# Performance work log

Measured on AMD Instinct MI355X. Metric: run time of the kernel, lower is better.

The kernel has to match this reference:

```python
import jax, jax.numpy as jnp
import numpy as np
from jax import lax

B, L, C = 128, 16384, 12      # batch, signal length, ECG channels
D = 128                        # latent_size
K, STRIDE = 64, 64             # encoder conv
TI, TO, TIG = 64, 8, 0         # timesteps_in / out / ignore


def setup_inputs() -> dict:
    key = jax.random.key(0)
    ks = jax.random.split(key, 7)
    s = 0.05
    X = jax.random.normal(ks[0], (B, L, C), jnp.float32)
    conv_w = jax.random.normal(ks[1], (D, C, K), jnp.float32) * s
    conv_b = jnp.zeros((D,), jnp.float32)
    W_ih = jax.random.normal(ks[2], (3 * D, D), jnp.float32) * s
    W_hh = jax.random.normal(ks[3], (3 * D, D), jnp.float32) * s
    b_ih = jnp.zeros((3 * D,), jnp.float32)
    b_hh = jnp.zeros((3 * D,), jnp.float32)
    pred_W = jax.random.normal(ks[4], (TO, D, D), jnp.float32) * s
    pred_b = jnp.zeros((TO, D), jnp.float32)
    return {"X": X, "conv_w": conv_w, "conv_b": conv_b, "W_ih": W_ih,
            "W_hh": W_hh, "b_ih": b_ih, "b_hh": b_hh,
            "pred_W": pred_W, "pred_b": pred_b}


def _gru(enc, W_ih, W_hh, b_ih, b_hh):
    # enc: [T, B, D] -> context [T, B, D], final hidden [B, D]
    def step(h, xt):
        gi = xt @ W_ih.T + b_ih              # [B, 3D]
        gh = h @ W_hh.T + b_hh
        ir, iz, inn = jnp.split(gi, 3, axis=-1)
        hr, hz, hn = jnp.split(gh, 3, axis=-1)
        r = jax.nn.sigmoid(ir + hr)
        z = jax.nn.sigmoid(iz + hz)
        n = jnp.tanh(inn + r * hn)
        h_new = (1.0 - z) * n + z * h
        return h_new, h_new
    h0 = jnp.zeros((enc.shape[1], enc.shape[2]), enc.dtype)
    hT, ctx = lax.scan(step, h0, enc)
    return ctx, hT


def reference(X, conv_w, conv_b, W_ih, W_hh, b_ih, b_hh, pred_W, pred_b):
    # X: [B, L, C] -> [B, C, L]
    x = X.transpose(0, 2, 1)
    z = lax.conv_general_dilated(x, conv_w, (STRIDE,), 'VALID',
                                 dimension_numbers=('NCH', 'OIH', 'NCH'))
    z = jax.nn.relu(z + conv_b[None, :, None])     # [B, D, T]
    enc = z.transpose(2, 0, 1)                     # [T, B, D]
    ctx, hT = _gru(enc, W_ih, W_hh, b_ih, b_hh)    # [T, B, D]

    T = enc.shape[0]
    S = T - TI - (TO + TIG + 1)                    # prediction steps per offset
    ctx_s = ctx[TI:TI + S]                         # [S, B, D]
    # predictor per offset i: ctx_s @ W[i].T + b[i]  -> [O, S, B, D]
    pred = jnp.einsum('sbd,oed->osbe', ctx_s, pred_W) + pred_b[:, None, None, :]
    # encoded targets enc[TI+i+1 : TI+i+1+S] for each offset i -> [O, S, B, D]
    idx = TI + 1 + jnp.arange(TO)[:, None] + jnp.arange(S)[None, :]
    tgt = enc[idx]
    # scores[o,s,b,c] = <encoded_latent[b], pred_latent[c]>
    scores = jnp.einsum('osbd,oscd->osbc', tgt, pred)
    logsm = jax.nn.log_softmax(scores, axis=-1)
    diag = jnp.diagonal(logsm, axis1=-2, axis2=-1)  # [O, S, B]
    denom = jnp.float32(B * TO * S)
    loss = -jnp.sum(diag) / denom
    correct = jnp.sum(jnp.argmax(logsm, axis=-2) == jnp.arange(B)[None, None, :])
    accuracy = correct.astype(jnp.float32) / denom
    hidden = hT[None]                               # [1, B, D]
    return accuracy, loss, hidden
```

## Files before the change

### kernel.cpp

```cpp
#include <hip/hip_runtime.h>
#include <math.h>

typedef __attribute__((ext_vector_type(8))) short bf16x8;
typedef __attribute__((ext_vector_type(4))) float f32x4;

#define Bdim 128
#define Cdim 12
#define Ddim 128
#define Tdim 256
#define TOn  8
#define TIn  64
#define Sn   183
#define DENOMF 187392.0f
#define NEG_INF -3.402823466e38f

#define OFFB_ENC 0
#define OFFB_CTX 8388608
#define OFFB_GI  16777216
#define OFFB_BCT 67108864
#define OFFB_WT  67305472
#define OFFB_LP  67403776
#define OFFB_CP  67409632
#define OFFB_WHP 67415488
#define OFFB_PWB 67513792

__device__ __forceinline__ float frcp(float x) { return __builtin_amdgcn_rcpf(x); }

__device__ __forceinline__ unsigned short f2b(float x) {
    unsigned int u = __builtin_bit_cast(unsigned int, x);
    u += 0x7FFFu + ((u >> 16) & 1u);
    return (unsigned short)(u >> 16);
}
__device__ __forceinline__ unsigned int pk2(float a, float b) {
    return (unsigned int)f2b(a) | ((unsigned int)f2b(b) << 16);
}

__device__ __forceinline__ uint4 ldg4u_pin(const unsigned int* p) {
    uint4 r;
    asm volatile("global_load_dwordx4 %0, %1, off\n\ts_waitcnt vmcnt(0)"
                 : "=v"(r) : "v"(p) : "memory");
    return r;
}

__device__ __forceinline__ void dot2b(float& acc, unsigned int a, unsigned int b) {
    asm("v_dot2_f32_bf16 %0, %1, %2, %0" : "+v"(acc) : "v"(a), "v"(b));
}

__device__ __forceinline__ float dpp_xor1(float x) {
    return __builtin_bit_cast(float, __builtin_amdgcn_mov_dpp(
        __builtin_bit_cast(int, x), 0xB1, 0xF, 0xF, true));
}
__device__ __forceinline__ float dpp_xor2(float x) {
    return __builtin_bit_cast(float, __builtin_amdgcn_mov_dpp(
        __builtin_bit_cast(int, x), 0x4E, 0xF, 0xF, true));
}

__global__ __launch_bounds__(256) void k_prep(const float* __restrict__ conv_w,
                                              unsigned short* __restrict__ BcT,
                                              const float* __restrict__ W_ih,
                                              unsigned short* __restrict__ Wt,
                                              const float* __restrict__ W_hh,
                                              unsigned int* __restrict__ Whp,
                                              const float* __restrict__ pW,
                                              unsigned short* __restrict__ pWb) {
    int id = blockIdx.x * 256 + threadIdx.x;
    if (id < 128 * 768) {
        int d = id / 768, klin = id % 768;
        int kt = klin / 12, c = klin % 12;
        BcT[id] = f2b(conv_w[d * 768 + c * 64 + kt]);
    }
    if (id < 384 * 128) Wt[id] = f2b(W_ih[id]);
    if (id < 384 * 64) {
        int row = id >> 6, k2 = id & 63;
        Whp[id] = pk2(W_hh[row * 128 + 2 * k2], W_hh[row * 128 + 2 * k2 + 1]);
    }
    if (id < 8 * 128 * 128) pWb[id] = f2b(pW[id]);
}

__global__ __launch_bounds__(256) void k_conv(const float* __restrict__ X,
                                              const unsigned short* __restrict__ BcT,
                                              const float* __restrict__ conv_b,
                                              unsigned short* __restrict__ encb) {
    const int t = blockIdx.x;
    __shared__ __align__(16) char As[16384];
    __shared__ __align__(16) char Bs[16384];
    const int tid = threadIdx.x;
    const int lane = tid & 63, wid = tid >> 6;
    const int wy = wid >> 1, wx = wid & 1;
    const int g = lane >> 4, ln = lane & 15;

    f32x4 acc[4][4];
#pragma unroll
    for (int i = 0; i < 4; ++i)
#pragma unroll
        for (int j = 0; j < 4; ++j) acc[i][j] = (f32x4){0.f, 0.f, 0.f, 0.f};

    for (int kc = 0; kc < 768; kc += 64) {
        __syncthreads();
#pragma unroll
        for (int it = 0; it < 4; ++it) {
            int G = tid + it * 256;
            int r = G >> 3, go = G & 7;
            const float* src = X + (size_t)r * (16384 * 12) + t * 768 + kc + go * 8;
            float4 f0 = *(const float4*)src;
            float4 f1 = *(const float4*)(src + 4);
            uint4 w; w.x = pk2(f0.x, f0.y); w.y = pk2(f0.z, f0.w);
            w.z = pk2(f1.x, f1.y); w.w = pk2(f1.z, f1.w);
            *(uint4*)(As + (r * 8 + (go ^ (r & 7))) * 16) = w;
            uint4 v = *(const uint4*)(BcT + (size_t)r * 768 + kc + go * 8);
            *(uint4*)(Bs + (r * 8 + (go ^ (r & 7))) * 16) = v;
        }
        __syncthreads();
#pragma unroll
        for (int ks = 0; ks < 2; ++ks) {
            bf16x8 af[4], bfr[4];
            const int kb = ks * 64 + g * 16;
#pragma unroll
            for (int mi = 0; mi < 4; ++mi) {
                int r = wy * 64 + mi * 16 + ln;
                af[mi] = *(const bf16x8*)(As + r * 128 + (kb ^ ((r & 7) << 4)));
            }
#pragma unroll
            for (int ni = 0; ni < 4; ++ni) {
                int r = wx * 64 + ni * 16 + ln;
                bfr[ni] = *(const bf16x8*)(Bs + r * 128 + (kb ^ ((r & 7) << 4)));
            }
#pragma unroll
            for (int mi = 0; mi < 4; ++mi)
#pragma unroll
                for (int ni = 0; ni < 4; ++ni)
                    acc[mi][ni] = __builtin_amdgcn_mfma_f32_16x16x32_bf16(af[mi], bfr[ni], acc[mi][ni], 0, 0, 0);
        }
    }
    float cb[4];
#pragma unroll
    for (int ni = 0; ni < 4; ++ni) cb[ni] = conv_b[wx * 64 + ni * 16 + ln];
    unsigned short* dst = encb + (size_t)t * (128 * 128);
#pragma unroll
    for (int mi = 0; mi < 4; ++mi)
#pragma unroll
        for (int jj = 0; jj < 4; ++jj) {
            int b = wy * 64 + mi * 16 + g * 4 + jj;
#pragma unroll
            for (int ni = 0; ni < 4; ++ni) {
                int d = wx * 64 + ni * 16 + ln;
                dst[b * 128 + d] = f2b(fmaxf(acc[mi][ni][jj] + cb[ni], 0.f));
            }
        }
}

__global__ __launch_bounds__(256) void k_gi(const unsigned short* __restrict__ encb,
                                            const unsigned short* __restrict__ Wt,
                                            const float* __restrict__ b_ih,
                                            const float* __restrict__ b_hh,
                                            float* __restrict__ gi) {
    const int mt = blockIdx.x, nt = blockIdx.y;
    __shared__ __align__(16) char As[32768];
    __shared__ __align__(16) char Bs[32768];
    const int tid = threadIdx.x;
    const int lane = tid & 63, wid = tid >> 6;
    const int wy = wid >> 1, wx = wid & 1;
    const int g = lane >> 4, ln = lane & 15;

    {
        const unsigned short* asrc = encb + (size_t)mt * (128 * 128);
        const unsigned short* bsrc = Wt + (size_t)nt * (128 * 128);
#pragma unroll
        for (int it = 0; it < 8; ++it) {
            int G = tid + it * 256;
            int r = G >> 4, go = G & 15;
            *(uint4*)(As + (r * 16 + (go ^ (r & 7))) * 16) = *(const uint4*)(asrc + r * 128 + go * 8);
            *(uint4*)(Bs + (r * 16 + (go ^ (r & 7))) * 16) = *(const uint4*)(bsrc + r * 128 + go * 8);
        }
    }
    __syncthreads();

    f32x4 acc[4][4];
#pragma unroll
    for (int i = 0; i < 4; ++i)
#pragma unroll
        for (int j = 0; j < 4; ++j) acc[i][j] = (f32x4){0.f, 0.f, 0.f, 0.f};
#pragma unroll
    for (int ks = 0; ks < 4; ++ks) {
        bf16x8 af[4], bfr[4];
        const int kb = ks * 64 + g * 16;
#pragma unroll
        for (int mi = 0; mi < 4; ++mi) {
            int r = wy * 64 + mi * 16 + ln;
            af[mi] = *(const bf16x8*)(As + r * 256 + (kb ^ ((r & 7) << 4)));
        }
#pragma unroll
        for (int ni = 0; ni < 4; ++ni) {
            int r = wx * 64 + ni * 16 + ln;
            bfr[ni] = *(const bf16x8*)(Bs + r * 256 + (kb ^ ((r & 7) << 4)));
        }
#pragma unroll
        for (int mi = 0; mi < 4; ++mi)
#pragma unroll
            for (int ni = 0; ni < 4; ++ni)
                acc[mi][ni] = __builtin_amdgcn_mfma_f32_16x16x32_bf16(af[mi], bfr[ni], acc[mi][ni], 0, 0, 0);
    }
    float bv[4];
#pragma unroll
    for (int ni = 0; ni < 4; ++ni) {
        int n = nt * 128 + wx * 64 + ni * 16 + ln;
        bv[ni] = b_ih[n] + (n < 256 ? b_hh[n] : 0.f);
    }
#pragma unroll
    for (int mi = 0; mi < 4; ++mi)
#pragma unroll
        for (int jj = 0; jj < 4; ++jj) {
            int m = mt * 128 + wy * 64 + mi * 16 + g * 4 + jj;
#pragma unroll
            for (int ni = 0; ni < 4; ++ni) {
                int n = nt * 128 + wx * 64 + ni * 16 + ln;
                gi[(size_t)m * 384 + n] = acc[mi][ni][jj] + bv[ni];
            }
        }
}

__global__ __launch_bounds__(512)
__attribute__((amdgpu_waves_per_eu(2, 2)))
void k_gru(const float* __restrict__ gi,
           const unsigned int* __restrict__ Whp,
           const float* __restrict__ bhh,
           unsigned short* __restrict__ ctxb,
           float* __restrict__ out_hidden) {
    const int b = blockIdx.x;
    const int tid = threadIdx.x;
    const int g = tid >> 2, q = tid & 3;
    __shared__ unsigned int hbuf[2][4][72];

    uint4 w0[4], w1[4], w2[4];
    {
        const unsigned int* W0 = Whp + (size_t)g * 64 + q * 16;
        const unsigned int* W1 = Whp + (size_t)(g + 128) * 64 + q * 16;
        const unsigned int* W2 = Whp + (size_t)(g + 256) * 64 + q * 16;
#pragma unroll
        for (int i = 0; i < 4; ++i) {
            w0[i] = ldg4u_pin(W0 + i * 4);
            w1[i] = ldg4u_pin(W1 + i * 4);
            w2[i] = ldg4u_pin(W2 + i * 4);
        }
    }
    const float bh2 = bhh[256 + g];

    if (!(g & 1)) hbuf[0][q][g >> 1] = 0u;

    float p0r = gi[(size_t)b * 384 + g];
    float p0z = gi[(size_t)b * 384 + 128 + g];
    float p0n = gi[(size_t)b * 384 + 256 + g];
    float p1r = gi[((size_t)128 + b) * 384 + g];
    float p1z = gi[((size_t)128 + b) * 384 + 128 + g];
    float p1n = gi[((size_t)128 + b) * 384 + 256 + g];
    float hold = 0.f;
    __syncthreads();

    for (int t = 0; t < 256; ++t) {
        const int cur = t & 1;
        float p2r = 0.f, p2z = 0.f, p2n = 0.f;
        if (t + 2 < 256) {
            const float* gp = gi + ((size_t)(t + 2) * 128 + b) * 384;
            p2r = gp[g]; p2z = gp[128 + g]; p2n = gp[256 + g];
        }

        const unsigned int* hc = &hbuf[cur][q][q * 16];
        uint4 h2[4];
#pragma unroll
        for (int i = 0; i < 4; ++i) h2[i] = *(const uint4*)(hc + i * 4);

        float a0 = 0.f, a1 = 0.f, a2 = 0.f, c0 = 0.f, c1 = 0.f, c2 = 0.f;
#pragma unroll
        for (int i = 0; i < 2; ++i) {
            dot2b(a0, w0[i].x, h2[i].x); dot2b(a1, w1[i].x, h2[i].x); dot2b(a2, w2[i].x, h2[i].x);
            dot2b(a0, w0[i].y, h2[i].y); dot2b(a1, w1[i].y, h2[i].y); dot2b(a2, w2[i].y, h2[i].y);
            dot2b(a0, w0[i].z, h2[i].z); dot2b(a1, w1[i].z, h2[i].z); dot2b(a2, w2[i].z, h2[i].z);
            dot2b(a0, w0[i].w, h2[i].w); dot2b(a1, w1[i].w, h2[i].w); dot2b(a2, w2[i].w, h2[i].w);
        }
#pragma unroll
        for (int i = 2; i < 4; ++i) {
            dot2b(c0, w0[i].x, h2[i].x); dot2b(c1, w1[i].x, h2[i].x); dot2b(c2, w2[i].x, h2[i].x);
            dot2b(c0, w0[i].y, h2[i].y); dot2b(c1, w1[i].y, h2[i].y); dot2b(c2, w2[i].y, h2[i].y);
            dot2b(c0, w0[i].z, h2[i].z); dot2b(c1, w1[i].z, h2[i].z); dot2b(c2, w2[i].z, h2[i].z);
            dot2b(c0, w0[i].w, h2[i].w); dot2b(c1, w1[i].w, h2[i].w); dot2b(c2, w2[i].w, h2[i].w);
        }
        a0 += c0; a1 += c1; a2 += c2;
        a0 += dpp_xor1(a0); a0 += dpp_xor2(a0);
        a1 += dpp_xor1(a1); a1 += dpp_xor2(a1);
        a2 += dpp_xor1(a2); a2 += dpp_xor2(a2);

        float r = frcp(1.f + __expf(-(p0r + a0)));
        float z = frcp(1.f + __expf(-(p0z + a1)));
        float xn = p0n + r * (a2 + bh2);
        xn = fmaxf(xn, -20.f);
        float e2 = __expf(-2.f * xn);
        float n = (1.f - e2) * frcp(1.f + e2);
        float hnew = (1.f - z) * n + z * hold;
        hold = hnew;

        ((unsigned short*)&hbuf[cur ^ 1][q][0])[g] = f2b(hnew);
        if (q == 0) {
            ctxb[((size_t)t * 128 + b) * 128 + g] = f2b(hnew);
            if (t == 255) out_hidden[b * 128 + g] = hnew;
        }
        p0r = p1r; p0z = p1z; p0n = p1n;
        p1r = p2r; p1z = p2z; p1n = p2n;
        asm volatile("s_waitcnt lgkmcnt(0)" ::: "memory");
        __builtin_amdgcn_s_barrier();
    }
}

__global__ __launch_bounds__(256) void k_cpc(const unsigned short* __restrict__ ctxb,
                                             const unsigned short* __restrict__ encb,
                                             const unsigned short* __restrict__ pWb,
                                             const float* __restrict__ pb,
                                             float* __restrict__ lp,
                                             float* __restrict__ cp) {
    const int o = blockIdx.x, s = blockIdx.y;
    __shared__ __align__(16) char bufA[32768];
    __shared__ __align__(16) char bufB[32768];
    __shared__ float rowm[2][128], rowsum[2][128];
    __shared__ float Lrow[128], diagv[128];
    __shared__ float colv[2][128];
    __shared__ int   colix[2][128];
    __shared__ float fin[4];

    const int tid = threadIdx.x;
    const int lane = tid & 63, wid = tid >> 6;
    const int wy = wid >> 1, wx = wid & 1;
    const int g = lane >> 4, ln = lane & 15;

    {
        const unsigned short* src = ctxb + (size_t)(TIn + s) * (128 * 128);
        const unsigned short* wsrc = pWb + (size_t)o * (128 * 128);
#pragma unroll
        for (int it = 0; it < 8; ++it) {
            int G = tid + it * 256;
            int r = G >> 4, go = G & 15;
            *(uint4*)(bufA + (r * 16 + (go ^ (r & 7))) * 16) = *(const uint4*)(src + r * 128 + go * 8);
            *(uint4*)(bufB + (r * 16 + (go ^ (r & 7))) * 16) = *(const uint4*)(wsrc + r * 128 + go * 8);
        }
    }
    __syncthreads();

    f32x4 acc[4][4];
#pragma unroll
    for (int i = 0; i < 4; ++i)
#pragma unroll
        for (int j = 0; j < 4; ++j) acc[i][j] = (f32x4){0.f, 0.f, 0.f, 0.f};
#pragma unroll
    for (int ks = 0; ks < 4; ++ks) {
        bf16x8 af[4], bfr[4];
        const int kb = ks * 64 + g * 16;
#pragma unroll
        for (int mi = 0; mi < 4; ++mi) {
            int r = wy * 64 + mi * 16 + ln;
            af[mi] = *(const bf16x8*)(bufB + r * 256 + (kb ^ ((r & 7) << 4)));
        }
#pragma unroll
        for (int ni = 0; ni < 4; ++ni) {
            int r = wx * 64 + ni * 16 + ln;
            bfr[ni] = *(const bf16x8*)(bufA + r * 256 + (kb ^ ((r & 7) << 4)));
        }
#pragma unroll
        for (int mi = 0; mi < 4; ++mi)
#pragma unroll
            for (int ni = 0; ni < 4; ++ni)
                acc[mi][ni] = __builtin_amdgcn_mfma_f32_16x16x32_bf16(af[mi], bfr[ni], acc[mi][ni], 0, 0, 0);
    }
    __syncthreads();

    {
        float pbv[4][4];
#pragma unroll
        for (int mi = 0; mi < 4; ++mi) {
            int e0 = wy * 64 + mi * 16 + g * 4;
#pragma unroll
            for (int jj = 0; jj < 4; ++jj) pbv[mi][jj] = pb[o * 128 + e0 + jj];
        }
#pragma unroll
        for (int mi = 0; mi < 4; ++mi) {
            int e0 = wy * 64 + mi * 16 + g * 4;
#pragma unroll
            for (int ni = 0; ni < 4; ++ni) {
                int c = wx * 64 + ni * 16 + ln;
                unsigned int lo = pk2(acc[mi][ni][0] + pbv[mi][0], acc[mi][ni][1] + pbv[mi][1]);
                unsigned int hi = pk2(acc[mi][ni][2] + pbv[mi][2], acc[mi][ni][3] + pbv[mi][3]);
                int byteoff = c * 256 + ((e0 * 2) ^ ((c & 7) << 4));
                *(uint2*)(bufB + byteoff) = make_uint2(lo, hi);
            }
        }
        const unsigned short* tsrc = encb + (size_t)(TIn + 1 + o + s) * (128 * 128);
#pragma unroll
        for (int it = 0; it < 8; ++it) {
            int G = tid + it * 256;
            int r = G >> 4, go = G & 15;
            *(uint4*)(bufA + (r * 16 + (go ^ (r & 7))) * 16) = *(const uint4*)(tsrc + r * 128 + go * 8);
        }
    }
    __syncthreads();

#pragma unroll
    for (int i = 0; i < 4; ++i)
#pragma unroll
        for (int j = 0; j < 4; ++j) acc[i][j] = (f32x4){0.f, 0.f, 0.f, 0.f};
#pragma unroll
    for (int ks = 0; ks < 4; ++ks) {
        bf16x8 af[4], bfr[4];
        const int kb = ks * 64 + g * 16;
#pragma unroll
        for (int mi = 0; mi < 4; ++mi) {
            int r = wy * 64 + mi * 16 + ln;
            af[mi] = *(const bf16x8*)(bufA + r * 256 + (kb ^ ((r & 7) << 4)));
        }
#pragma unroll
        for (int ni = 0; ni < 4; ++ni) {
            int r = wx * 64 + ni * 16 + ln;
            bfr[ni] = *(const bf16x8*)(bufB + r * 256 + (kb ^ ((r & 7) << 4)));
        }
#pragma unroll
        for (int mi = 0; mi < 4; ++mi)
#pragma unroll
            for (int ni = 0; ni < 4; ++ni)
                acc[mi][ni] = __builtin_amdgcn_mfma_f32_16x16x32_bf16(af[mi], bfr[ni], acc[mi][ni], 0, 0, 0);
    }

#pragma unroll
    for (int mi = 0; mi < 4; ++mi) {
#pragma unroll
        for (int jj = 0; jj < 4; ++jj) {
            float m = fmaxf(fmaxf(acc[mi][0][jj], acc[mi][1][jj]),
                            fmaxf(acc[mi][2][jj], acc[mi][3][jj]));
            m = fmaxf(m, __shfl_xor(m, 1)); m = fmaxf(m, __shfl_xor(m, 2));
            m = fmaxf(m, __shfl_xor(m, 4)); m = fmaxf(m, __shfl_xor(m, 8));
            float sm = __expf(acc[mi][0][jj] - m) + __expf(acc[mi][1][jj] - m)
                     + __expf(acc[mi][2][jj] - m) + __expf(acc[mi][3][jj] - m);
            sm += __shfl_xor(sm, 1); sm += __shfl_xor(sm, 2);
            sm += __shfl_xor(sm, 4); sm += __shfl_xor(sm, 8);
            int b = wy * 64 + mi * 16 + g * 4 + jj;
            if (ln == 0) { rowm[wx][b] = m; rowsum[wx][b] = sm; }
            if (wy == wx && ln == g * 4 + jj) diagv[b] = acc[mi][mi][jj];
        }
    }
    __syncthreads();
    if (tid < 128) {
        float m0 = rowm[0][tid], m1 = rowm[1][tid];
        float mm = fmaxf(m0, m1);
        float ss = rowsum[0][tid] * __expf(m0 - mm) + rowsum[1][tid] * __expf(m1 - mm);
        Lrow[tid] = mm + __logf(ss);
    }
    __syncthreads();

    float Lr[4][4];
#pragma unroll
    for (int mi = 0; mi < 4; ++mi)
#pragma unroll
        for (int jj = 0; jj < 4; ++jj) Lr[mi][jj] = Lrow[wy * 64 + mi * 16 + g * 4 + jj];

#pragma unroll
    for (int ni = 0; ni < 4; ++ni) {
        float best = NEG_INF; int bidx = 0x7fffffff;
#pragma unroll
        for (int mi = 0; mi < 4; ++mi)
#pragma unroll
            for (int jj = 0; jj < 4; ++jj) {
                float v = acc[mi][ni][jj] - Lr[mi][jj];
                int r = wy * 64 + mi * 16 + g * 4 + jj;
                if (v > best) { best = v; bidx = r; }
            }
#pragma unroll
        for (int mask = 16; mask <= 32; mask <<= 1) {
            float ov = __shfl_xor(best, mask);
            int   oi = __shfl_xor(bidx, mask);
            if (ov > best || (ov == best && oi < bidx)) { best = ov; bidx = oi; }
        }
        if (g == 0) {
            int c = wx * 64 + ni * 16 + ln;
            colv[wy][c] = best; colix[wy][c] = bidx;
        }
    }
    __syncthreads();

    float lsum = 0.f, csum = 0.f;
    if (tid < 128) {
        lsum = diagv[tid] - Lrow[tid];
        float v0 = colv[0][tid], v1 = colv[1][tid];
        int ix = (v1 > v0) ? colix[1][tid] : colix[0][tid];
        csum = (ix == tid) ? 1.f : 0.f;
    }
#pragma unroll
    for (int off = 32; off > 0; off >>= 1) {
        lsum += __shfl_down(lsum, off);
        csum += __shfl_down(csum, off);
    }
    if (lane == 0 && wid < 2) { fin[wid] = lsum; fin[2 + wid] = csum; }
    __syncthreads();
    if (tid == 0) {
        lp[o * Sn + s] = fin[0] + fin[1];
        cp[o * Sn + s] = fin[2] + fin[3];
    }
}

__global__ __launch_bounds__(256) void k_final(const float* __restrict__ lp,
                                               const float* __restrict__ cp,
                                               float* __restrict__ out) {
    __shared__ float sl[256], sc2[256];
    const int tid = threadIdx.x;
    float l = 0.f, c = 0.f;
    for (int i = tid; i < TOn * Sn; i += 256) { l += lp[i]; c += cp[i]; }
    sl[tid] = l; sc2[tid] = c;
    __syncthreads();
    for (int s = 128; s > 0; s >>= 1) {
        if (tid < s) { sl[tid] += sl[tid + s]; sc2[tid] += sc2[tid + s]; }
        __syncthreads();
    }
    if (tid == 0) {
        out[0] = sc2[0] / DENOMF;
        out[1] = -sl[0] / DENOMF;
    }
}

extern "C" void kernel_launch(void* const* d_in, const int* in_sizes, int n_in,
                              void* d_out, int out_size, void* d_ws, size_t ws_size,
                              hipStream_t stream) {
    const float* X      = (const float*)d_in[0];
    const float* conv_w = (const float*)d_in[1];
    const float* conv_b = (const float*)d_in[2];
    const float* W_ih   = (const float*)d_in[3];
    const float* W_hh   = (const float*)d_in[4];
    const float* b_ih   = (const float*)d_in[5];
    const float* b_hh   = (const float*)d_in[6];
    const float* pred_W = (const float*)d_in[7];
    const float* pred_b = (const float*)d_in[8];
    float* out = (float*)d_out;
    char*  ws  = (char*)d_ws;

    unsigned short* encb = (unsigned short*)(ws + OFFB_ENC);
    unsigned short* ctxb = (unsigned short*)(ws + OFFB_CTX);
    float*          gi   = (float*)(ws + OFFB_GI);
    unsigned short* BcT  = (unsigned short*)(ws + OFFB_BCT);
    unsigned short* Wt   = (unsigned short*)(ws + OFFB_WT);
    float*          lp   = (float*)(ws + OFFB_LP);
    float*          cp   = (float*)(ws + OFFB_CP);
    unsigned int*   Whp  = (unsigned int*)(ws + OFFB_WHP);
    unsigned short* pWb  = (unsigned short*)(ws + OFFB_PWB);

    k_prep <<<dim3(512),     dim3(256), 0, stream>>>(conv_w, BcT, W_ih, Wt, W_hh, Whp, pred_W, pWb);
    k_conv <<<dim3(256),     dim3(256), 0, stream>>>(X, BcT, conv_b, encb);
    k_gi   <<<dim3(256, 3),  dim3(256), 0, stream>>>(encb, Wt, b_ih, b_hh, gi);
    k_gru  <<<dim3(128),     dim3(512), 0, stream>>>(gi, Whp, b_hh, ctxb, out + 2);
    k_cpc  <<<dim3(TOn, Sn), dim3(256), 0, stream>>>(ctxb, encb, pWb, pred_b, lp, cp);
    k_final<<<dim3(1),       dim3(256), 0, stream>>>(lp, cp, out);
}
```

Baseline: 230.0 us.

## Compute GRU recurrent matvec with MFMA over 16-batch tiles

```diff
diff --git a/kernel.cpp b/kernel.cpp
--- a/kernel.cpp
+++ b/kernel.cpp
@@ -40,19 +40,6 @@
     asm volatile("global_load_dwordx4 %0, %1, off\n\ts_waitcnt vmcnt(0)"
                  : "=v"(r) : "v"(p) : "memory");
     return r;
-}
-
-__device__ __forceinline__ void dot2b(float& acc, unsigned int a, unsigned int b) {
-    asm("v_dot2_f32_bf16 %0, %1, %2, %0" : "+v"(acc) : "v"(a), "v"(b));
-}
-
-__device__ __forceinline__ float dpp_xor1(float x) {
-    return __builtin_bit_cast(float, __builtin_amdgcn_mov_dpp(
-        __builtin_bit_cast(int, x), 0xB1, 0xF, 0xF, true));
-}
-__device__ __forceinline__ float dpp_xor2(float x) {
-    return __builtin_bit_cast(float, __builtin_amdgcn_mov_dpp(
-        __builtin_bit_cast(int, x), 0x4E, 0xF, 0xF, true));
 }
 
 __global__ __launch_bounds__(256) void k_prep(const float* __restrict__ conv_w,
@@ -153,7 +140,7 @@
                                             const unsigned short* __restrict__ Wt,
                                             const float* __restrict__ b_ih,
                                             const float* __restrict__ b_hh,
-                                            float* __restrict__ gi) {
+                                            float* __restrict__ gi2) {
     const int mt = blockIdx.x, nt = blockIdx.y;
     __shared__ __align__(16) char As[32768];
     __shared__ __align__(16) char Bs[32768];
@@ -209,105 +196,98 @@
 #pragma unroll
     for (int mi = 0; mi < 4; ++mi)
 #pragma unroll
-        for (int jj = 0; jj < 4; ++jj) {
-            int m = mt * 128 + wy * 64 + mi * 16 + g * 4 + jj;
-#pragma unroll
-            for (int ni = 0; ni < 4; ++ni) {
-                int n = nt * 128 + wx * 64 + ni * 16 + ln;
-                gi[(size_t)m * 384 + n] = acc[mi][ni][jj] + bv[ni];
-            }
+        for (int ni = 0; ni < 4; ++ni) {
+            int gout = wx * 64 + ni * 16 + ln;
+            int brow = wy * 64 + mi * 16 + g * 4;
+            float4 st;
+            st.x = acc[mi][ni][0] + bv[ni];
+            st.y = acc[mi][ni][1] + bv[ni];
+            st.z = acc[mi][ni][2] + bv[ni];
+            st.w = acc[mi][ni][3] + bv[ni];
+            *(float4*)(gi2 + ((size_t)(mt * 3 + nt) * 128 + gout) * 128 + brow) = st;
         }
 }
 
 __global__ __launch_bounds__(512)
 __attribute__((amdgpu_waves_per_eu(2, 2)))
-void k_gru(const float* __restrict__ gi,
+void k_gru(const float* __restrict__ gi2,
            const unsigned int* __restrict__ Whp,
            const float* __restrict__ bhh,
            unsigned short* __restrict__ ctxb,
            float* __restrict__ out_hidden) {
-    const int b = blockIdx.x;
+    const int bb = blockIdx.x;
     const int tid = threadIdx.x;
-    const int g = tid >> 2, q = tid & 3;
-    __shared__ unsigned int hbuf[2][4][72];
-
-    uint4 w0[4], w1[4], w2[4];
-    {
-        const unsigned int* W0 = Whp + (size_t)g * 64 + q * 16;
-        const unsigned int* W1 = Whp + (size_t)(g + 128) * 64 + q * 16;
-        const unsigned int* W2 = Whp + (size_t)(g + 256) * 64 + q * 16;
-#pragma unroll
-        for (int i = 0; i < 4; ++i) {
-            w0[i] = ldg4u_pin(W0 + i * 4);
-            w1[i] = ldg4u_pin(W1 + i * 4);
-            w2[i] = ldg4u_pin(W2 + i * 4);
-        }
+    const int w = tid >> 6, l = tid & 63;
+    const int gl = l & 15, q = l >> 4;
+    const int g = w * 16 + gl;
+    __shared__ __align__(16) char hlds[2][4096];
+
+    bf16x8 bR[4], bZ[4], bN[4];
+#pragma unroll
+    for (int kt = 0; kt < 4; ++kt) {
+        bR[kt] = __builtin_bit_cast(bf16x8, ldg4u_pin(Whp + (size_t)(g) * 64 + kt * 16 + q * 4));
+        bZ[kt] = __builtin_bit_cast(bf16x8, ldg4u_pin(Whp + (size_t)(128 + g) * 64 + kt * 16 + q * 4));
+        bN[kt] = __builtin_bit_cast(bf16x8, ldg4u_pin(Whp + (size_t)(256 + g) * 64 + kt * 16 + q * 4));
     }
     const float bh2 = bhh[256 + g];
 
-    if (!(g & 1)) hbuf[0][q][g >> 1] = 0u;
-
-    float p0r = gi[(size_t)b * 384 + g];
-    float p0z = gi[(size_t)b * 384 + 128 + g];
-    float p0n = gi[(size_t)b * 384 + 256 + g];
-    float p1r = gi[((size_t)128 + b) * 384 + g];
-    float p1z = gi[((size_t)128 + b) * 384 + 128 + g];
-    float p1n = gi[((size_t)128 + b) * 384 + 256 + g];
-    float hold = 0.f;
+    if (tid < 256) *(uint4*)(hlds[0] + tid * 16) = (uint4){0u, 0u, 0u, 0u};
+
+    const float* gbase = gi2 + (size_t)(bb * 16 + q * 4);
+#define GI_PTR(T, G) (gbase + ((size_t)((T) * 3 + (G)) * 128 + g) * 128)
+    f32x4 gR0 = *(const f32x4*)GI_PTR(0, 0), gZ0 = *(const f32x4*)GI_PTR(0, 1), gN0 = *(const f32x4*)GI_PTR(0, 2);
+    f32x4 gR1 = *(const f32x4*)GI_PTR(1, 0), gZ1 = *(const f32x4*)GI_PTR(1, 1), gN1 = *(const f32x4*)GI_PTR(1, 2);
+    float hold[4] = {0.f, 0.f, 0.f, 0.f};
     __syncthreads();
 
     for (int t = 0; t < 256; ++t) {
         const int cur = t & 1;
-        float p2r = 0.f, p2z = 0.f, p2n = 0.f;
+        f32x4 gR2 = (f32x4){0.f,0.f,0.f,0.f}, gZ2 = gR2, gN2 = gR2;
         if (t + 2 < 256) {
-            const float* gp = gi + ((size_t)(t + 2) * 128 + b) * 384;
-            p2r = gp[g]; p2z = gp[128 + g]; p2n = gp[256 + g];
-        }
-
-        const unsigned int* hc = &hbuf[cur][q][q * 16];
-        uint4 h2[4];
-#pragma unroll
-        for (int i = 0; i < 4; ++i) h2[i] = *(const uint4*)(hc + i * 4);
-
-        float a0 = 0.f, a1 = 0.f, a2 = 0.f, c0 = 0.f, c1 = 0.f, c2 = 0.f;
-#pragma unroll
-        for (int i = 0; i < 2; ++i) {
-            dot2b(a0, w0[i].x, h2[i].x); dot2b(a1, w1[i].x, h2[i].x); dot2b(a2, w2[i].x, h2[i].x);
-            dot2b(a0, w0[i].y, h2[i].y); dot2b(a1, w1[i].y, h2[i].y); dot2b(a2, w2[i].y, h2[i].y);
-            dot2b(a0, w0[i].z, h2[i].z); dot2b(a1, w1[i].z, h2[i].z); dot2b(a2, w2[i].z, h2[i].z);
-            dot2b(a0, w0[i].w, h2[i].w); dot2b(a1, w1[i].w, h2[i].w); dot2b(a2, w2[i].w, h2[i].w);
-        }
-#pragma unroll
-        for (int i = 2; i < 4; ++i) {
-            dot2b(c0, w0[i].x, h2[i].x); dot2b(c1, w1[i].x, h2[i].x); dot2b(c2, w2[i].x, h2[i].x);
-            dot2b(c0, w0[i].y, h2[i].y); dot2b(c1, w1[i].y, h2[i].y); dot2b(c2, w2[i].y, h2[i].y);
-            dot2b(c0, w0[i].z, h2[i].z); dot2b(c1, w1[i].z, h2[i].z); dot2b(c2, w2[i].z, h2[i].z);
-            dot2b(c0, w0[i].w, h2[i].w); dot2b(c1, w1[i].w, h2[i].w); dot2b(c2, w2[i].w, h2[i].w);
-        }
-        a0 += c0; a1 += c1; a2 += c2;
-        a0 += dpp_xor1(a0); a0 += dpp_xor2(a0);
-        a1 += dpp_xor1(a1); a1 += dpp_xor2(a1);
-        a2 += dpp_xor1(a2); a2 += dpp_xor2(a2);
-
-        float r = frcp(1.f + __expf(-(p0r + a0)));
-        float z = frcp(1.f + __expf(-(p0z + a1)));
-        float xn = p0n + r * (a2 + bh2);
-        xn = fmaxf(xn, -20.f);
-        float e2 = __expf(-2.f * xn);
-        float n = (1.f - e2) * frcp(1.f + e2);
-        float hnew = (1.f - z) * n + z * hold;
-        hold = hnew;
-
-        ((unsigned short*)&hbuf[cur ^ 1][q][0])[g] = f2b(hnew);
-        if (q == 0) {
-            ctxb[((size_t)t * 128 + b) * 128 + g] = f2b(hnew);
-            if (t == 255) out_hidden[b * 128 + g] = hnew;
-        }
-        p0r = p1r; p0z = p1z; p0n = p1n;
-        p1r = p2r; p1z = p2z; p1n = p2n;
+            gR2 = *(const f32x4*)GI_PTR(t + 2, 0);
+            gZ2 = *(const f32x4*)GI_PTR(t + 2, 1);
+            gN2 = *(const f32x4*)GI_PTR(t + 2, 2);
+        }
+
+        const char* hcur = hlds[cur];
+        bf16x8 af[4];
+#pragma unroll
+        for (int kt = 0; kt < 4; ++kt)
+            af[kt] = *(const bf16x8*)(hcur + gl * 256 + ((kt * 64 + q * 16) ^ ((gl & 7) << 4)));
+
+        f32x4 aR = gR0, aZ = gZ0;
+        f32x4 aN = (f32x4){bh2, bh2, bh2, bh2};
+#pragma unroll
+        for (int kt = 0; kt < 4; ++kt) {
+            aR = __builtin_amdgcn_mfma_f32_16x16x32_bf16(af[kt], bR[kt], aR, 0, 0, 0);
+            aZ = __builtin_amdgcn_mfma_f32_16x16x32_bf16(af[kt], bZ[kt], aZ, 0, 0, 0);
+            aN = __builtin_amdgcn_mfma_f32_16x16x32_bf16(af[kt], bN[kt], aN, 0, 0, 0);
+        }
+
+        char* hnxt = hlds[cur ^ 1];
+#pragma unroll
+        for (int jj = 0; jj < 4; ++jj) {
+            float r = frcp(1.f + __expf(-aR[jj]));
+            float z = frcp(1.f + __expf(-aZ[jj]));
+            float xn = gN0[jj] + r * aN[jj];
+            xn = fmaxf(xn, -20.f);
+            float e2 = __expf(-2.f * xn);
+            float n = (1.f - e2) * frcp(1.f + e2);
+            float hnew = (1.f - z) * n + z * hold[jj];
+            hold[jj] = hnew;
+            const int brow = q * 4 + jj;
+            unsigned short hb = f2b(hnew);
+            *(unsigned short*)(hnxt + brow * 256 + ((g * 2) ^ ((brow & 7) << 4))) = hb;
+            ctxb[((size_t)t * 128 + bb * 16 + brow) * 128 + g] = hb;
+            if (t == 255) out_hidden[(bb * 16 + brow) * 128 + g] = hnew;
+        }
+
+        gR0 = gR1; gZ0 = gZ1; gN0 = gN1;
+        gR1 = gR2; gZ1 = gZ2; gN1 = gN2;
         asm volatile("s_waitcnt lgkmcnt(0)" ::: "memory");
         __builtin_amdgcn_s_barrier();
     }
+#undef GI_PTR
 }
 
 __global__ __launch_bounds__(256) void k_cpc(const unsigned short* __restrict__ ctxb,
@@ -537,7 +517,7 @@
 
     unsigned short* encb = (unsigned short*)(ws + OFFB_ENC);
     unsigned short* ctxb = (unsigned short*)(ws + OFFB_CTX);
-    float*          gi   = (float*)(ws + OFFB_GI);
+    float*          gi2  = (float*)(ws + OFFB_GI);
     unsigned short* BcT  = (unsigned short*)(ws + OFFB_BCT);
     unsigned short* Wt   = (unsigned short*)(ws + OFFB_WT);
     float*          lp   = (float*)(ws + OFFB_LP);
@@ -547,8 +527,8 @@
 
     k_prep <<<dim3(512),     dim3(256), 0, stream>>>(conv_w, BcT, W_ih, Wt, W_hh, Whp, pred_W, pWb);
     k_conv <<<dim3(256),     dim3(256), 0, stream>>>(X, BcT, conv_b, encb);
-    k_gi   <<<dim3(256, 3),  dim3(256), 0, stream>>>(encb, Wt, b_ih, b_hh, gi);
-    k_gru  <<<dim3(128),     dim3(512), 0, stream>>>(gi, Whp, b_hh, ctxb, out + 2);
+    k_gi   <<<dim3(256, 3),  dim3(256), 0, stream>>>(encb, Wt, b_ih, b_hh, gi2);
+    k_gru  <<<dim3(8),       dim3(512), 0, stream>>>(gi2, Whp, b_hh, ctxb, out + 2);
     k_cpc  <<<dim3(TOn, Sn), dim3(256), 0, stream>>>(ctxb, encb, pWb, pred_b, lp, cp);
     k_final<<<dim3(1),       dim3(256), 0, stream>>>(lp, cp, out);
 }
```

New measurement: 371.7 us. 1.62x slower.
